# Performance work log

Hardware: AMD Instinct MI355X
Metric: run time of the kernel (lower is better)

The kernel has to match this reference:

```python
import jax, jax.numpy as jnp
import numpy as np
import math

DIM = 96
NUM_HEADS = 8
MLP_RATIO = 4.0

def _coord_encoding(h, w, scale, d_model):
    # matches HierarchicalCoordinateEncoding: per freq i, channels are
    # [sin(cell_y), cos(cell_y), sin(cell_x), cos(cell_x), sin(y), cos(y), sin(x), cos(x)]
    y = jnp.arange(h, dtype=jnp.float32) / (h - 1)
    x = jnp.arange(w, dtype=jnp.float32) / (w - 1)
    yy, xx = jnp.meshgrid(y, x, indexing='ij')
    yf = yy.reshape(-1)
    xf = xx.reshape(-1)
    cs = 2.0 / scale
    coords4 = jnp.stack([yf * cs, xf * cs, yf, xf], axis=-1)  # [N,4]
    nf = d_model // 8
    freqs = (2.0 ** jnp.arange(nf, dtype=jnp.float32)) * math.pi  # [nf]
    phase = coords4[:, None, :] * freqs[None, :, None]  # [N,nf,4]
    enc = jnp.stack([jnp.sin(phase), jnp.cos(phase)], axis=-1)  # [N,nf,4,2]
    return enc.reshape(h * w, nf * 8)  # [N,d_model] (d_model divisible by 8)

def _layernorm(x, g, b, eps=1e-5):
    mu = jnp.mean(x, axis=-1, keepdims=True)
    var = jnp.var(x, axis=-1, keepdims=True)
    return (x - mu) * jax.lax.rsqrt(var + eps) * g + b

def setup_inputs():
    key = jax.random.key(0)
    ks = jax.random.split(key, 8)
    B, C, H, W = 8, DIM, 96, 96
    hid = int(DIM * MLP_RATIO)
    std = 0.02
    return {
        'features': jax.random.normal(ks[0], (B, C, H, W), jnp.float32),
        'scale': 2,
        'mlp1_w1': jax.random.normal(ks[1], (2 * DIM, hid), jnp.float32) * std,
        'mlp1_b1': jnp.zeros((hid,), jnp.float32),
        'mlp1_w2': jax.random.normal(ks[2], (hid, DIM), jnp.float32) * std,
        'mlp1_b2': jnp.zeros((DIM,), jnp.float32),
        'norm1_g': jnp.ones((DIM,), jnp.float32),
        'norm1_b': jnp.zeros((DIM,), jnp.float32),
        'qkv_w': jax.random.normal(ks[3], (DIM, 3 * DIM), jnp.float32) * std,
        'proj_w': jax.random.normal(ks[4], (DIM, DIM), jnp.float32) * std,
        'proj_b': jnp.zeros((DIM,), jnp.float32),
        'norm2_g': jnp.ones((DIM,), jnp.float32),
        'norm2_b': jnp.zeros((DIM,), jnp.float32),
        'mlp2_w1': jax.random.normal(ks[5], (DIM, hid), jnp.float32) * std,
        'mlp2_b1': jnp.zeros((hid,), jnp.float32),
        'mlp2_w2': jax.random.normal(ks[6], (hid, 3), jnp.float32) * std,
        'mlp2_b2': jnp.zeros((3,), jnp.float32),
    }

def reference(features, scale, mlp1_w1, mlp1_b1, mlp1_w2, mlp1_b2, norm1_g, norm1_b, qkv_w, proj_w, proj_b, norm2_g, norm2_b, mlp2_w1, mlp2_b1, mlp2_w2, mlp2_b2):
    B, C, H_lr, W_lr = features.shape
    H, W = int(H_lr * scale), int(W_lr * scale)
    N = H * W
    nh = NUM_HEADS
    hd = C // nh
    ce = _coord_encoding(H, W, float(scale), C)  # [N,C]
    # bilinear upsample, half-pixel centers == torch align_corners=False
    feat_up = jax.image.resize(features, (B, C, H, W), method='linear')
    feat_flat = feat_up.transpose(0, 2, 3, 1).reshape(B, N, C)
    combined = jnp.concatenate([feat_flat, jnp.broadcast_to(ce[None], (B, N, C))], axis=-1)  # [B,N,2C]
    x = jax.nn.gelu(combined @ mlp1_w1 + mlp1_b1, approximate=False) @ mlp1_w2 + mlp1_b2  # [B,N,C]
    x = _layernorm(x, norm1_g, norm1_b)
    # linear attention: softmax over q feature dim and k token dim
    qkv = (x @ qkv_w).reshape(B, N, 3, nh, hd).transpose(2, 0, 3, 1, 4)  # [3,B,nh,N,hd]
    q, k, v = qkv[0], qkv[1], qkv[2]
    q = jax.nn.softmax(q, axis=-1) * (hd ** -0.5)
    k = jax.nn.softmax(k, axis=-2)
    ctx = jnp.einsum('bhnd,bhne->bhde', k, v)  # [B,nh,hd,hd]
    attn = jnp.einsum('bhnd,bhde->bhne', q, ctx)  # [B,nh,N,hd]
    attn = attn.transpose(0, 2, 1, 3).reshape(B, N, C)
    x = x + (attn @ proj_w + proj_b)
    x = _layernorm(x, norm2_g, norm2_b)
    rgb = jax.nn.gelu(x @ mlp2_w1 + mlp2_b1, approximate=False) @ mlp2_w2 + mlp2_b2  # [B,N,3]
    rgb = rgb.reshape(B, H, W, 3).transpose(0, 3, 1, 2)  # [B,3,H,W]
    return jnp.clip(jnp.tanh(rgb) * 0.5 + 0.5, 0.0, 1.0)
```

## Files before the change

kernel.cpp:

```cpp
#include <hip/hip_runtime.h>
#include <math.h>

typedef unsigned short u16;
typedef unsigned int   u32;
typedef unsigned long long u64;
typedef __bf16  bf16x8 __attribute__((ext_vector_type(8)));
typedef short   s16x8  __attribute__((ext_vector_type(8)));
typedef float   f32x4  __attribute__((ext_vector_type(4)));

#define NTOK 36864
#define TTOT (8*NTOK)

__device__ __forceinline__ f32x4 mfma16(s16x8 a, s16x8 b, f32x4 c){
  return __builtin_amdgcn_mfma_f32_16x16x32_bf16(
      __builtin_bit_cast(bf16x8, a), __builtin_bit_cast(bf16x8, b), c, 0, 0, 0);
}
__device__ __forceinline__ int swz(int row, int bc, int stride){
  return row*stride + (bc ^ ((row&7)<<4));
}
__device__ __forceinline__ u16 f2bf(float f){
  u32 u = __float_as_uint(f);
  return (u16)((u + 0x7fffu + ((u>>16)&1u)) >> 16);
}
__device__ __forceinline__ u32 pk2f(float a, float b){
  return (u32)f2bf(a) | ((u32)f2bf(b)<<16);
}
__device__ __forceinline__ u64 pk4f(float a, float b, float c, float d){
  return (u64)pk2f(a,b) | ((u64)pk2f(c,d)<<32);
}
__device__ __forceinline__ float bf2f(u16 h){ return __uint_as_float(((u32)h)<<16); }
__device__ __forceinline__ float rcp_(float x){ return __builtin_amdgcn_rcpf(x); }

__device__ __forceinline__ float gelu_(float x){
  float z = fabsf(x) * 0.70710678118654752f;
  float t = rcp_(1.0f + 0.3275911f*z);
  float poly = t*(0.254829592f + t*(-0.284496736f + t*(1.421413741f + t*(-1.453152027f + t*1.061405429f))));
  float e = __expf(-z*z);
  float erf = 1.0f - poly*e;
  erf = (x < 0.0f) ? -erf : erf;
  return 0.5f*x*(1.0f + erf);
}
__device__ __forceinline__ float tanhf_(float x){
  float e = __expf(2.0f*x);
  return 1.0f - 2.0f*rcp_(e + 1.0f);
}

#define LDSF(arr, row, kc, stride) (*(const s16x8*)((const char*)(arr) + swz((row),(kc)*2,(stride))))

__global__ void prep_w(const float* __restrict__ w1, const float* __restrict__ w2,
                       const float* __restrict__ qkvw, const float* __restrict__ projw,
                       const float* __restrict__ m2w1, const float* __restrict__ m2w2,
                       u16* __restrict__ w1t, u16* __restrict__ w2t,
                       u16* __restrict__ wqt, u16* __restrict__ wkt, u16* __restrict__ wvt,
                       u16* __restrict__ pjt, u16* __restrict__ m2w1t, u16* __restrict__ m2w2t)
{
  int i = blockIdx.x*256 + threadIdx.x;
  if (i < 73728){ int n=i/192, k=i%192; w1t[i] = f2bf(w1[k*384+n]); return; }
  i -= 73728;
  if (i < 36864){ int n=i/384, k=i%384; w2t[i] = f2bf(w2[k*96+n]); return; }
  i -= 36864;
  if (i < 9216){ int n=i/96, k=i%96; wqt[i] = f2bf(qkvw[k*288+n]); return; }
  i -= 9216;
  if (i < 9216){ int n=i/96, k=i%96; wkt[i] = f2bf(qkvw[k*288+96+n]); return; }
  i -= 9216;
  if (i < 9216){ int n=i/96, k=i%96; wvt[i] = f2bf(qkvw[k*288+192+n]); return; }
  i -= 9216;
  if (i < 9216){ int n=i/96, k=i%96; pjt[i] = f2bf(projw[k*96+n]); return; }
  i -= 9216;
  if (i < 36864){ int n=i/96, k=i%96; m2w1t[i] = f2bf(m2w1[k*384+n]); return; }
  i -= 36864;
  if (i < 6144){ int n=i/384, k=i%384; m2w2t[i] = (n<3)? f2bf(m2w2[k*3+n]) : (u16)0; return; }
}

__global__ void prep_feat(const float* __restrict__ feat, u16* __restrict__ featcl){
  __shared__ u16 t[96*100];
  const int tid = threadIdx.x;
  const int b = blockIdx.x/96, y = blockIdx.x%96;
  for (int i=tid; i<9216; i+=256){
    int c = i/96, x = i%96;
    t[c*100+x] = f2bf(feat[((size_t)(b*96+c)*96 + y)*96 + x]);
  }
  __syncthreads();
  for (int i=tid; i<9216; i+=256){
    int x = i/96, c = i%96;
    featcl[(((size_t)b*96 + y)*96 + x)*96 + c] = t[c*100+x];
  }
}

__global__ void prep_ce(u16* __restrict__ ce){
  int gid = blockIdx.x*256 + threadIdx.x;
  if (gid >= 36864*48) return;
  int n = gid/48, c2 = gid%48;
  int row = n/192, col = n%192;
  int fi = c2>>2, cs = c2&3;
  float coord = ((cs&1)==0) ? (float)row*(1.0f/191.0f) : (float)col*(1.0f/191.0f);
  float u = coord * (float)(1<<fi);
  u = u - 2.0f*floorf(u*0.5f);
  float ph = u * 3.14159265358979323846f;
  float s, c;
  __sincosf(ph, &s, &c);
  *(u32*)(ce + (size_t)n*96 + c2*2) = pk2f(s, c);
}

__global__ __launch_bounds__(256,3) void k1(
    const u16* __restrict__ featcl, const u16* __restrict__ ce,
    const u16* __restrict__ w1t, const float* __restrict__ b1,
    const u16* __restrict__ w2t, const float* __restrict__ b2,
    const float* __restrict__ g1, const float* __restrict__ be1,
    const u16* __restrict__ wkt, const u16* __restrict__ wvt,
    u16* __restrict__ x1, float* __restrict__ ctx_un)
{
  __shared__ u16 comb[64*192];
  __shared__ char scratch[26624];
  const int tid = threadIdx.x, w = tid>>6, lane = tid&63, kg = lane>>4, ln = lane&15;
  const int bi = blockIdx.x;
  const int b = bi/576, rem = bi%576, ty = rem/24, tx = rem%24;
  u16* hid  = (u16*)scratch;
  u16* ektp = (u16*)scratch;
  u16* vtp  = (u16*)(scratch + 12288);

  for (int i=tid; i<1024; i+=256){
    int rr = 96 + (i>>6), t = i&63;
    *(u16*)((char*)vtp + swz(rr, t*2, 128)) = (rr==96) ? (u16)0x3f80 : (u16)0;
  }

  {
    const u16* fbase = featcl + (size_t)b*884736;
    const int l = tid>>2, cg = tid&3;
    int row = ty*8 + (l>>3), col = tx*8 + (l&7);
    float fy = row*0.5f - 0.25f;
    int y0 = (int)floorf(fy); float dy = fy - (float)y0;
    int y0c = max(y0,0), y1c = min(y0+1,95);
    float fx = col*0.5f - 0.25f;
    int x0 = (int)floorf(fx); float dx = fx - (float)x0;
    int x0c = max(x0,0), x1c = min(x0+1,95);
    float w00=(1.f-dy)*(1.f-dx), w01=(1.f-dy)*dx, w10=dy*(1.f-dx), w11=dy*dx;
    const u16* p00 = fbase + (size_t)(y0c*96+x0c)*96;
    const u16* p01 = fbase + (size_t)(y0c*96+x1c)*96;
    const u16* p10 = fbase + (size_t)(y1c*96+x0c)*96;
    const u16* p11 = fbase + (size_t)(y1c*96+x1c)*96;
    #pragma unroll
    for (int j=0; j<12; ++j){
      int c2 = cg*12 + j;
      u32 u00 = *(const u32*)(p00 + c2*2), u01 = *(const u32*)(p01 + c2*2);
      u32 u10 = *(const u32*)(p10 + c2*2), u11 = *(const u32*)(p11 + c2*2);
      float a0 = w00*bf2f((u16)u00) + w01*bf2f((u16)u01)
               + w10*bf2f((u16)u10) + w11*bf2f((u16)u11);
      float a1 = w00*bf2f((u16)(u00>>16)) + w01*bf2f((u16)(u01>>16))
               + w10*bf2f((u16)(u10>>16)) + w11*bf2f((u16)(u11>>16));
      *(u32*)((char*)comb + swz(l, c2*4, 384)) = pk2f(a0, a1);
    }
  }
  for (int i=tid; i<64*12; i+=256){
    int l = i/12, sg = i%12;
    int n = (ty*8+(l>>3))*192 + tx*8 + (l&7);
    *(s16x8*)((char*)comb + swz(l, 192 + sg*16, 384)) = *(const s16x8*)(ce + (size_t)n*96 + sg*8);
  }
  __syncthreads();

  f32x4 a2[6] = {};
  for (int h=0; h<2; ++h){
    f32x4 acc[3][4] = {};
    #pragma unroll
    for (int ks=0; ks<6; ++ks){
      s16x8 af[3];
      #pragma unroll
      for (int nf=0; nf<3; ++nf)
        af[nf] = *(const s16x8*)(w1t + (size_t)(192*h+48*w+16*nf+ln)*192 + ks*32+8*kg);
      #pragma unroll
      for (int tf=0; tf<4; ++tf){
        s16x8 bfr = LDSF(comb, 16*tf+ln, ks*32+8*kg, 384);
        #pragma unroll
        for (int nf=0; nf<3; ++nf) acc[nf][tf] = mfma16(af[nf], bfr, acc[nf][tf]);
      }
    }
    #pragma unroll
    for (int nf=0; nf<3; ++nf){
      int lc0 = 48*w + 16*nf + 4*kg;
      float4 bb = *(const float4*)(b1 + 192*h + lc0);
      #pragma unroll
      for (int tf=0; tf<4; ++tf){
        int token = 16*tf + ln;
        u64 v = pk4f(gelu_(acc[nf][tf][0]+bb.x), gelu_(acc[nf][tf][1]+bb.y),
                     gelu_(acc[nf][tf][2]+bb.z), gelu_(acc[nf][tf][3]+bb.w));
        *(u64*)((char*)hid + swz(token, lc0*2, 384)) = v;
      }
    }
    __syncthreads();
    #pragma unroll
    for (int ks=0; ks<6; ++ks){
      s16x8 af = LDSF(hid, 16*w+ln, ks*32+8*kg, 384);
      #pragma unroll
      for (int nf=0; nf<6; ++nf){
        s16x8 bfr = *(const s16x8*)(w2t + (size_t)(16*nf+ln)*384 + 192*h + ks*32+8*kg);
        a2[nf] = mfma16(af, bfr, a2[nf]);
      }
    }
    if (h==0) __syncthreads();
  }

  float gg[6], bbv[6];
  #pragma unroll
  for (int nf=0; nf<6; ++nf){
    int col = 16*nf + ln;
    float bias = b2[col];
    gg[nf] = g1[col]; bbv[nf] = be1[col];
    #pragma unroll
    for (int r=0; r<4; ++r) a2[nf][r] += bias;
  }
  __syncthreads();
  #pragma unroll
  for (int r=0; r<4; ++r){
    float s=0.f, sq=0.f;
    #pragma unroll
    for (int nf=0; nf<6; ++nf){ float v=a2[nf][r]; s+=v; sq+=v*v; }
    #pragma unroll
    for (int m=8; m; m>>=1){ s += __shfl_xor(s,m); sq += __shfl_xor(sq,m); }
    float mean = s*(1.f/96.f);
    float var  = sq*(1.f/96.f) - mean*mean;
    float rstd = rsqrtf(var + 1e-5f);
    int trow = 16*w + 4*kg + r;
    #pragma unroll
    for (int nf=0; nf<6; ++nf){
      float o = (a2[nf][r]-mean)*rstd*gg[nf] + bbv[nf];
      *(u16*)((char*)comb + swz(trow, (16*nf+ln)*2, 256)) = f2bf(o);
    }
  }
  __syncthreads();

  for (int i=tid; i<64*12; i+=256){
    int l = i/12, sg = i%12;
    s16x8 v = *(const s16x8*)((const char*)comb + swz(l, sg*16, 256));
    int n = (ty*8+(l>>3))*192 + tx*8 + (l&7);
    *(s16x8*)(x1 + ((size_t)b*NTOK + n)*96 + sg*8) = v;
  }

  {
    f32x4 ka[6] = {}, va[6] = {};
    #pragma unroll
    for (int ks=0; ks<3; ++ks){
      s16x8 xb = LDSF(comb, 16*w+ln, ks*32+8*kg, 256);
      #pragma unroll
      for (int mf=0; mf<6; ++mf){
        s16x8 ak = *(const s16x8*)(wkt + (size_t)(16*mf+ln)*96 + ks*32+8*kg);
        s16x8 av = *(const s16x8*)(wvt + (size_t)(16*mf+ln)*96 + ks*32+8*kg);
        ka[mf] = mfma16(ak, xb, ka[mf]);
        va[mf] = mfma16(av, xb, va[mf]);
      }
    }
    #pragma unroll
    for (int mf=0; mf<6; ++mf){
      #pragma unroll
      for (int r=0; r<4; ++r){
        int d = 16*mf + 4*kg + r;
        int tok = 16*w + ln;
        *(u16*)((char*)ektp + swz(d, tok*2, 128)) = f2bf(__expf(ka[mf][r]));
        *(u16*)((char*)vtp  + swz(d, tok*2, 128)) = f2bf(va[mf][r]);
      }
    }
  }
  __syncthreads();

  {
    const int tmi[20] = {0,0,1,1,1,2,2,3,3,4,4,4,5,5, 0,1,2,3,4,5};
    const int tni[20] = {0,1,0,1,2,1,2,3,4,3,4,5,4,5, 6,6,6,6,6,6};
    f32x4 c5[5] = {};
    #pragma unroll
    for (int t=0; t<20; ++t){
      if (t/5 == w){
        #pragma unroll
        for (int grp=0; grp<2; ++grp){
          s16x8 ea = LDSF(ektp, 16*tmi[t]+ln, 32*grp+8*kg, 128);
          s16x8 vb = LDSF(vtp,  16*tni[t]+ln, 32*grp+8*kg, 128);
          c5[t%5] = mfma16(ea, vb, c5[t%5]);
        }
      }
    }
    #pragma unroll
    for (int t=0; t<20; ++t){
      if (t/5 == w){
        #pragma unroll
        for (int r=0; r<4; ++r){
          int d = 16*tmi[t] + 4*kg + r;
          if (tni[t]==6){
            if (ln==0) atomicAdd(&ctx_un[(b*96+d)*112 + 96], c5[t%5][r]);
          } else {
            int e = 16*tni[t] + ln;
            if (d/12 == e/12) atomicAdd(&ctx_un[(b*96+d)*112 + e], c5[t%5][r]);
          }
        }
      }
    }
  }
}

__global__ void k2c(const float* __restrict__ ctx_un, float* __restrict__ ctxc){
  int i = blockIdx.x*256 + threadIdx.x;
  if (i < 8*1152){
    int b = i/1152, rr = i%1152, h = rr/144, de = rr%144, d = de/12, e = de%12;
    int dg = h*12+d, eg = h*12+e;
    ctxc[i] = ctx_un[(b*96+dg)*112 + eg] / ctx_un[(b*96+dg)*112 + 96];
  }
}

__global__ __launch_bounds__(256,2) void k3(
    const u16* __restrict__ x1, const u16* __restrict__ wqt, const u16* __restrict__ pjt,
    const float* __restrict__ projb, const float* __restrict__ g2, const float* __restrict__ be2,
    const u16* __restrict__ m2w1t, const float* __restrict__ m2b1,
    const u16* __restrict__ m2w2t, const float* __restrict__ m2b2,
    const float* __restrict__ ctxc, float* __restrict__ out)
{
  __shared__ u16 bufA[128*128];
  __shared__ u16 bufB[128*128];
  __shared__ float ctxsh[8*145];
  __shared__ float rgbsh[3][128];
  const int tid = threadIdx.x, w = tid>>6, lane = tid&63, kg = lane>>4, ln = lane&15;
  const int bi = blockIdx.x, b = bi/288;
  const size_t t0 = (size_t)bi*128;
  const int n0 = (bi%288)*128;

  for (int i=tid; i<1152; i+=256){
    int h = i/144, rem = i%144;
    ctxsh[h*145 + rem] = ctxc[b*1152 + i];
  }

  {
    f32x4 q[6][2] = {};
    #pragma unroll
    for (int ks=0; ks<3; ++ks){
      s16x8 af[6];
      #pragma unroll
      for (int nf=0; nf<6; ++nf)
        af[nf] = *(const s16x8*)(wqt + (size_t)(16*nf+ln)*96 + ks*32+8*kg);
      #pragma unroll
      for (int tf=0; tf<2; ++tf){
        s16x8 bfr = *(const s16x8*)(x1 + (t0 + 32*w + 16*tf + ln)*96 + ks*32+8*kg);
        #pragma unroll
        for (int nf=0; nf<6; ++nf) q[nf][tf] = mfma16(af[nf], bfr, q[nf][tf]);
      }
    }
    #pragma unroll
    for (int nf=0; nf<6; ++nf){
      #pragma unroll
      for (int tf=0; tf<2; ++tf){
        int token = 32*w + 16*tf + ln;
        u64 v = pk4f(q[nf][tf][0], q[nf][tf][1], q[nf][tf][2], q[nf][tf][3]);
        *(u64*)((char*)bufA + swz(token, (16*nf+4*kg)*2, 256)) = v;
      }
    }
  }
  __syncthreads();

  const float scl = 0.28867513459481287f;
  for (int p=tid; p<128*8; p+=256){
    int tok = p>>3, h = p&7;
    const float* cb = &ctxsh[h*145];
    float ex[12], ssum = 0.f;
    #pragma unroll
    for (int d=0; d<12; ++d){
      float qv = bf2f(*(const u16*)((const char*)bufA + swz(tok, (h*12+d)*2, 256)));
      ex[d] = __expf(qv); ssum += ex[d];
    }
    float inv = scl*rcp_(ssum);
    float av[12];
    #pragma unroll
    for (int e=0; e<12; ++e){
      float a = 0.f;
      #pragma unroll
      for (int d=0; d<12; ++d) a += ex[d]*cb[d*12+e];
      av[e] = a*inv;
    }
    #pragma unroll
    for (int e2=0; e2<6; e2+=2){
      u64 v = pk4f(av[2*e2], av[2*e2+1], av[2*e2+2], av[2*e2+3]);
      *(u64*)((char*)bufB + swz(tok, (h*12+2*e2)*2, 256)) = v;
    }
  }
  __syncthreads();

  f32x4 p[2][6] = {};
  #pragma unroll
  for (int ks=0; ks<3; ++ks){
    s16x8 a[2];
    #pragma unroll
    for (int mi=0; mi<2; ++mi) a[mi] = LDSF(bufB, 16*(2*w+mi)+ln, ks*32+8*kg, 256);
    #pragma unroll
    for (int nf=0; nf<6; ++nf){
      s16x8 bfr = *(const s16x8*)(pjt + (size_t)(16*nf+ln)*96 + ks*32+8*kg);
      #pragma unroll
      for (int mi=0; mi<2; ++mi) p[mi][nf] = mfma16(a[mi], bfr, p[mi][nf]);
    }
  }
  {
    float gg[6], bbv[6], pb[6];
    #pragma unroll
    for (int nf=0; nf<6; ++nf){
      int col = 16*nf + ln;
      pb[nf] = projb[col]; gg[nf] = g2[col]; bbv[nf] = be2[col];
    }
    #pragma unroll
    for (int mi=0; mi<2; ++mi){
      #pragma unroll
      for (int r=0; r<4; ++r){
        int trow = 16*(2*w+mi)+4*kg+r;
        float vv[6]; float s=0.f, sq=0.f;
        #pragma unroll
        for (int nf=0; nf<6; ++nf){
          float xv = bf2f(x1[(t0 + trow)*96 + 16*nf+ln]);
          float v = p[mi][nf][r] + pb[nf] + xv;
          vv[nf] = v; s += v; sq += v*v;
        }
        #pragma unroll
        for (int m=8; m; m>>=1){ s += __shfl_xor(s,m); sq += __shfl_xor(sq,m); }
        float mean = s*(1.f/96.f);
        float var  = sq*(1.f/96.f) - mean*mean;
        float rstd = rsqrtf(var + 1e-5f);
        #pragma unroll
        for (int nf=0; nf<6; ++nf){
          float o = (vv[nf]-mean)*rstd*gg[nf] + bbv[nf];
          *(u16*)((char*)bufA + swz(trow, (16*nf+ln)*2, 256)) = f2bf(o);
        }
      }
    }
  }

  f32x4 rgb[2] = {};
  for (int nc=0; nc<4; ++nc){
    f32x4 hh[6][2] = {};
    #pragma unroll
    for (int ks=0; ks<3; ++ks){
      s16x8 af[6];
      #pragma unroll
      for (int nf=0; nf<6; ++nf)
        af[nf] = *(const s16x8*)(m2w1t + (size_t)(nc*96+16*nf+ln)*96 + ks*32+8*kg);
      #pragma unroll
      for (int tf=0; tf<2; ++tf){
        s16x8 bfr = LDSF(bufA, 32*w+16*tf+ln, ks*32+8*kg, 256);
        #pragma unroll
        for (int nf=0; nf<6; ++nf) hh[nf][tf] = mfma16(af[nf], bfr, hh[nf][tf]);
      }
    }
    #pragma unroll
    for (int nf=0; nf<6; ++nf){
      int hc0 = nc*96 + 16*nf + 4*kg;
      float4 bb = *(const float4*)(m2b1 + hc0);
      #pragma unroll
      for (int tf=0; tf<2; ++tf){
        int token = 32*w + 16*tf + ln;
        u64 v = pk4f(gelu_(hh[nf][tf][0]+bb.x), gelu_(hh[nf][tf][1]+bb.y),
                     gelu_(hh[nf][tf][2]+bb.z), gelu_(hh[nf][tf][3]+bb.w));
        *(u64*)((char*)bufB + swz(token, (16*nf+4*kg)*2, 256)) = v;
      }
    }
    #pragma unroll
    for (int ks=0; ks<3; ++ks){
      s16x8 bfr = *(const s16x8*)(m2w2t + (size_t)ln*384 + nc*96 + ks*32 + 8*kg);
      #pragma unroll
      for (int mi=0; mi<2; ++mi){
        s16x8 a = LDSF(bufB, 16*(2*w+mi)+ln, ks*32+8*kg, 256);
        rgb[mi] = mfma16(a, bfr, rgb[mi]);
      }
    }
  }
  if (ln < 3){
    float bias = m2b2[ln];
    #pragma unroll
    for (int mi=0; mi<2; ++mi)
      #pragma unroll
      for (int r=0; r<4; ++r){
        int trow = 16*(2*w+mi)+4*kg+r;
        float v = tanhf_(rgb[mi][r] + bias)*0.5f + 0.5f;
        v = fminf(fmaxf(v, 0.f), 1.f);
        rgbsh[ln][trow] = v;
      }
  }
  __syncthreads();
  for (int i=tid; i<384; i+=256){
    int ch = i>>7, t = i&127;
    out[((size_t)(b*3+ch))*NTOK + n0 + t] = rgbsh[ch][t];
  }
}

extern "C" void kernel_launch(void* const* d_in, const int* in_sizes, int n_in,
                              void* d_out, int out_size, void* d_ws, size_t ws_size,
                              hipStream_t stream)
{
  (void)in_sizes; (void)n_in; (void)out_size; (void)ws_size;
  const float* feat  = (const float*)d_in[0];
  const float* m1w1  = (const float*)d_in[2];
  const float* m1b1  = (const float*)d_in[3];
  const float* m1w2  = (const float*)d_in[4];
  const float* m1b2  = (const float*)d_in[5];
  const float* n1g   = (const float*)d_in[6];
  const float* n1b   = (const float*)d_in[7];
  const float* qkvw  = (const float*)d_in[8];
  const float* projw = (const float*)d_in[9];
  const float* projb = (const float*)d_in[10];
  const float* n2g   = (const float*)d_in[11];
  const float* n2b   = (const float*)d_in[12];
  const float* m2w1  = (const float*)d_in[13];
  const float* m2b1  = (const float*)d_in[14];
  const float* m2w2  = (const float*)d_in[15];
  const float* m2b2  = (const float*)d_in[16];
  float* out = (float*)d_out;

  char* p = (char*)d_ws;
  auto bump = [&](size_t bytes)->char*{
    char* r = p;
    p += (bytes + 255) & ~(size_t)255;
    return r;
  };
  u16*  x1     = (u16*) bump((size_t)TTOT*96*2);
  u16*  featcl = (u16*) bump((size_t)8*96*96*96*2);
  u16*  ce     = (u16*) bump((size_t)NTOK*96*2);
  u16*  w1t    = (u16*) bump(73728*2);
  u16*  w2t    = (u16*) bump(36864*2);
  u16*  wqt    = (u16*) bump(9216*2);
  u16*  wkt    = (u16*) bump(9216*2);
  u16*  wvt    = (u16*) bump(9216*2);
  u16*  pjt    = (u16*) bump(9216*2);
  u16*  m2w1t  = (u16*) bump(36864*2);
  u16*  m2w2t  = (u16*) bump(6144*2);
  float* ctx_un= (float*)bump((size_t)8*96*112*4);
  float* ctxc  = (float*)bump((size_t)8*1152*4);

  hipLaunchKernelGGL(prep_w, dim3(744), dim3(256), 0, stream,
                     m1w1, m1w2, qkvw, projw, m2w1, m2w2,
                     w1t, w2t, wqt, wkt, wvt, pjt, m2w1t, m2w2t);
  hipLaunchKernelGGL(prep_feat, dim3(768), dim3(256), 0, stream, feat, featcl);
  hipLaunchKernelGGL(prep_ce, dim3(6912), dim3(256), 0, stream, ce);
  hipMemsetAsync(ctx_un, 0, (size_t)8*96*112*4, stream);
  hipLaunchKernelGGL(k1, dim3(4608), dim3(256), 0, stream,
                     featcl, ce, w1t, m1b1, w2t, m1b2, n1g, n1b, wkt, wvt, x1, ctx_un);
  hipLaunchKernelGGL(k2c, dim3(36), dim3(256), 0, stream, ctx_un, ctxc);
  hipLaunchKernelGGL(k3, dim3(2304), dim3(256), 0, stream,
                     x1, wqt, pjt, projb, n2g, n2b, m2w1t, m2b1, m2w2t, m2b2, ctxc, out);
}
```

Baseline: 498.6 us.

## Make k1 MLP wave-local over token rows to drop barriers and shrink LDS

The first-MLP stage now gives each wave its own 16-token row block. The hidden dimension is processed in four 96-wide chunks, so the GELU intermediate stays wave-private and needs no block barriers. This removes several __syncthreads and cuts shared memory (the hidden buffer shrinks and the K/V transposes are aliased onto the comb buffer), which allows raising launch bounds to 4 blocks per CU. In exchange, each wave now loads all first-layer weight fragments from global/L2 rather than sharing them across the block's token tiles, which adds weight traffic and register pressure.

```diff
diff --git a/kernel.cpp b/kernel.cpp
--- a/kernel.cpp
+++ b/kernel.cpp
@@ -102,7 +102,7 @@
   *(u32*)(ce + (size_t)n*96 + c2*2) = pk2f(s, c);
 }
 
-__global__ __launch_bounds__(256,3) void k1(
+__global__ __launch_bounds__(256,4) void k1(
     const u16* __restrict__ featcl, const u16* __restrict__ ce,
     const u16* __restrict__ w1t, const float* __restrict__ b1,
     const u16* __restrict__ w2t, const float* __restrict__ b2,
@@ -111,18 +111,13 @@
     u16* __restrict__ x1, float* __restrict__ ctx_un)
 {
   __shared__ u16 comb[64*192];
-  __shared__ char scratch[26624];
+  __shared__ u16 hid[64*128];
   const int tid = threadIdx.x, w = tid>>6, lane = tid&63, kg = lane>>4, ln = lane&15;
   const int bi = blockIdx.x;
   const int b = bi/576, rem = bi%576, ty = rem/24, tx = rem%24;
-  u16* hid  = (u16*)scratch;
-  u16* ektp = (u16*)scratch;
-  u16* vtp  = (u16*)(scratch + 12288);
-
-  for (int i=tid; i<1024; i+=256){
-    int rr = 96 + (i>>6), t = i&63;
-    *(u16*)((char*)vtp + swz(rr, t*2, 128)) = (rr==96) ? (u16)0x3f80 : (u16)0;
-  }
+  char* ektB = (char*)comb;
+  char* vtB  = (char*)comb + 12288;
+  char* vhiB = (char*)hid;
 
   {
     const u16* fbase = featcl + (size_t)b*884736;
@@ -151,112 +146,116 @@
       *(u32*)((char*)comb + swz(l, c2*4, 384)) = pk2f(a0, a1);
     }
   }
-  for (int i=tid; i<64*12; i+=256){
-    int l = i/12, sg = i%12;
-    int n = (ty*8+(l>>3))*192 + tx*8 + (l&7);
-    *(s16x8*)((char*)comb + swz(l, 192 + sg*16, 384)) = *(const s16x8*)(ce + (size_t)n*96 + sg*8);
+  {
+    int row = 16*w + (lane>>2);
+    int n = (ty*8+(row>>3))*192 + tx*8 + (row&7);
+    int sg0 = (lane&3)*3;
+    #pragma unroll
+    for (int j=0; j<3; ++j){
+      int sg = sg0+j;
+      *(s16x8*)((char*)comb + swz(row, 192 + sg*16, 384)) = *(const s16x8*)(ce + (size_t)n*96 + sg*8);
+    }
+  }
+
+  f32x4 a2[6] = {};
+  #pragma unroll
+  for (int q=0; q<4; ++q){
+    f32x4 acc[6] = {};
+    #pragma unroll
+    for (int ks=0; ks<6; ++ks){
+      s16x8 bfr = LDSF(comb, 16*w+ln, ks*32+8*kg, 384);
+      #pragma unroll
+      for (int nf=0; nf<6; ++nf){
+        s16x8 af = *(const s16x8*)(w1t + (size_t)(96*q+16*nf+ln)*192 + ks*32+8*kg);
+        acc[nf] = mfma16(af, bfr, acc[nf]);
+      }
+    }
+    #pragma unroll
+    for (int nf=0; nf<6; ++nf){
+      int lc0 = 16*nf + 4*kg;
+      float4 bb = *(const float4*)(b1 + 96*q + lc0);
+      u64 v = pk4f(gelu_(acc[nf][0]+bb.x), gelu_(acc[nf][1]+bb.y),
+                   gelu_(acc[nf][2]+bb.z), gelu_(acc[nf][3]+bb.w));
+      *(u64*)((char*)hid + swz(16*w+ln, lc0*2, 256)) = v;
+    }
+    #pragma unroll
+    for (int ks=0; ks<3; ++ks){
+      s16x8 af = LDSF(hid, 16*w+ln, ks*32+8*kg, 256);
+      #pragma unroll
+      for (int nf=0; nf<6; ++nf){
+        s16x8 bfr = *(const s16x8*)(w2t + (size_t)(16*nf+ln)*384 + 96*q + ks*32+8*kg);
+        a2[nf] = mfma16(af, bfr, a2[nf]);
+      }
+    }
+  }
+
+  {
+    float gg[6], bbv[6];
+    #pragma unroll
+    for (int nf=0; nf<6; ++nf){
+      int col = 16*nf + ln;
+      float bias = b2[col];
+      gg[nf] = g1[col]; bbv[nf] = be1[col];
+      #pragma unroll
+      for (int r=0; r<4; ++r) a2[nf][r] += bias;
+    }
+    #pragma unroll
+    for (int r=0; r<4; ++r){
+      float s=0.f, sq=0.f;
+      #pragma unroll
+      for (int nf=0; nf<6; ++nf){ float v=a2[nf][r]; s+=v; sq+=v*v; }
+      #pragma unroll
+      for (int m=8; m; m>>=1){ s += __shfl_xor(s,m); sq += __shfl_xor(sq,m); }
+      float mean = s*(1.f/96.f);
+      float var  = sq*(1.f/96.f) - mean*mean;
+      float rstd = rsqrtf(var + 1e-5f);
+      int trow = 16*w + 4*kg + r;
+      #pragma unroll
+      for (int nf=0; nf<6; ++nf){
+        float o = (a2[nf][r]-mean)*rstd*gg[nf] + bbv[nf];
+        *(u16*)((char*)comb + swz(trow, (16*nf+ln)*2, 384)) = f2bf(o);
+      }
+    }
+  }
+
+  {
+    int row = 16*w + (lane>>2);
+    int n = (ty*8+(row>>3))*192 + tx*8 + (row&7);
+    int sg0 = (lane&3)*3;
+    #pragma unroll
+    for (int j=0; j<3; ++j){
+      int sg = sg0+j;
+      s16x8 v = *(const s16x8*)((const char*)comb + swz(row, sg*16, 384));
+      *(s16x8*)(x1 + ((size_t)b*NTOK + n)*96 + sg*8) = v;
+    }
+  }
+
+  f32x4 ka[6] = {}, va[6] = {};
+  #pragma unroll
+  for (int ks=0; ks<3; ++ks){
+    s16x8 xb = LDSF(comb, 16*w+ln, ks*32+8*kg, 384);
+    #pragma unroll
+    for (int mf=0; mf<6; ++mf){
+      s16x8 akf = *(const s16x8*)(wkt + (size_t)(16*mf+ln)*96 + ks*32+8*kg);
+      s16x8 avf = *(const s16x8*)(wvt + (size_t)(16*mf+ln)*96 + ks*32+8*kg);
+      ka[mf] = mfma16(akf, xb, ka[mf]);
+      va[mf] = mfma16(avf, xb, va[mf]);
+    }
   }
   __syncthreads();
 
-  f32x4 a2[6] = {};
-  for (int h=0; h<2; ++h){
-    f32x4 acc[3][4] = {};
-    #pragma unroll
-    for (int ks=0; ks<6; ++ks){
-      s16x8 af[3];
-      #pragma unroll
-      for (int nf=0; nf<3; ++nf)
-        af[nf] = *(const s16x8*)(w1t + (size_t)(192*h+48*w+16*nf+ln)*192 + ks*32+8*kg);
-      #pragma unroll
-      for (int tf=0; tf<4; ++tf){
-        s16x8 bfr = LDSF(comb, 16*tf+ln, ks*32+8*kg, 384);
-        #pragma unroll
-        for (int nf=0; nf<3; ++nf) acc[nf][tf] = mfma16(af[nf], bfr, acc[nf][tf]);
-      }
-    }
-    #pragma unroll
-    for (int nf=0; nf<3; ++nf){
-      int lc0 = 48*w + 16*nf + 4*kg;
-      float4 bb = *(const float4*)(b1 + 192*h + lc0);
-      #pragma unroll
-      for (int tf=0; tf<4; ++tf){
-        int token = 16*tf + ln;
-        u64 v = pk4f(gelu_(acc[nf][tf][0]+bb.x), gelu_(acc[nf][tf][1]+bb.y),
-                     gelu_(acc[nf][tf][2]+bb.z), gelu_(acc[nf][tf][3]+bb.w));
-        *(u64*)((char*)hid + swz(token, lc0*2, 384)) = v;
-      }
-    }
-    __syncthreads();
-    #pragma unroll
-    for (int ks=0; ks<6; ++ks){
-      s16x8 af = LDSF(hid, 16*w+ln, ks*32+8*kg, 384);
-      #pragma unroll
-      for (int nf=0; nf<6; ++nf){
-        s16x8 bfr = *(const s16x8*)(w2t + (size_t)(16*nf+ln)*384 + 192*h + ks*32+8*kg);
-        a2[nf] = mfma16(af, bfr, a2[nf]);
-      }
-    }
-    if (h==0) __syncthreads();
-  }
-
-  float gg[6], bbv[6];
+  for (int i=tid; i<1024; i+=256){
+    int rr = i>>6, t = i&63;
+    *(u16*)(vhiB + swz(rr, t*2, 128)) = (rr==0) ? (u16)0x3f80 : (u16)0;
+  }
   #pragma unroll
-  for (int nf=0; nf<6; ++nf){
-    int col = 16*nf + ln;
-    float bias = b2[col];
-    gg[nf] = g1[col]; bbv[nf] = be1[col];
-    #pragma unroll
-    for (int r=0; r<4; ++r) a2[nf][r] += bias;
-  }
-  __syncthreads();
-  #pragma unroll
-  for (int r=0; r<4; ++r){
-    float s=0.f, sq=0.f;
-    #pragma unroll
-    for (int nf=0; nf<6; ++nf){ float v=a2[nf][r]; s+=v; sq+=v*v; }
-    #pragma unroll
-    for (int m=8; m; m>>=1){ s += __shfl_xor(s,m); sq += __shfl_xor(sq,m); }
-    float mean = s*(1.f/96.f);
-    float var  = sq*(1.f/96.f) - mean*mean;
-    float rstd = rsqrtf(var + 1e-5f);
-    int trow = 16*w + 4*kg + r;
-    #pragma unroll
-    for (int nf=0; nf<6; ++nf){
-      float o = (a2[nf][r]-mean)*rstd*gg[nf] + bbv[nf];
-      *(u16*)((char*)comb + swz(trow, (16*nf+ln)*2, 256)) = f2bf(o);
-    }
-  }
-  __syncthreads();
-
-  for (int i=tid; i<64*12; i+=256){
-    int l = i/12, sg = i%12;
-    s16x8 v = *(const s16x8*)((const char*)comb + swz(l, sg*16, 256));
-    int n = (ty*8+(l>>3))*192 + tx*8 + (l&7);
-    *(s16x8*)(x1 + ((size_t)b*NTOK + n)*96 + sg*8) = v;
-  }
-
-  {
-    f32x4 ka[6] = {}, va[6] = {};
-    #pragma unroll
-    for (int ks=0; ks<3; ++ks){
-      s16x8 xb = LDSF(comb, 16*w+ln, ks*32+8*kg, 256);
-      #pragma unroll
-      for (int mf=0; mf<6; ++mf){
-        s16x8 ak = *(const s16x8*)(wkt + (size_t)(16*mf+ln)*96 + ks*32+8*kg);
-        s16x8 av = *(const s16x8*)(wvt + (size_t)(16*mf+ln)*96 + ks*32+8*kg);
-        ka[mf] = mfma16(ak, xb, ka[mf]);
-        va[mf] = mfma16(av, xb, va[mf]);
-      }
-    }
-    #pragma unroll
-    for (int mf=0; mf<6; ++mf){
-      #pragma unroll
-      for (int r=0; r<4; ++r){
-        int d = 16*mf + 4*kg + r;
-        int tok = 16*w + ln;
-        *(u16*)((char*)ektp + swz(d, tok*2, 128)) = f2bf(__expf(ka[mf][r]));
-        *(u16*)((char*)vtp  + swz(d, tok*2, 128)) = f2bf(va[mf][r]);
-      }
+  for (int mf=0; mf<6; ++mf){
+    #pragma unroll
+    for (int r=0; r<4; ++r){
+      int d = 16*mf + 4*kg + r;
+      int tok = 16*w + ln;
+      *(u16*)(ektB + swz(d, tok*2, 128)) = f2bf(__expf(ka[mf][r]));
+      *(u16*)(vtB  + swz(d, tok*2, 128)) = f2bf(va[mf][r]);
     }
   }
   __syncthreads();
@@ -270,8 +269,10 @@
       if (t/5 == w){
         #pragma unroll
         for (int grp=0; grp<2; ++grp){
-          s16x8 ea = LDSF(ektp, 16*tmi[t]+ln, 32*grp+8*kg, 128);
-          s16x8 vb = LDSF(vtp,  16*tni[t]+ln, 32*grp+8*kg, 128);
+          s16x8 ea = *(const s16x8*)(ektB + swz(16*tmi[t]+ln, (32*grp+8*kg)*2, 128));
+          s16x8 vb = (tni[t]==6)
+            ? *(const s16x8*)(vhiB + swz(ln, (32*grp+8*kg)*2, 128))
+            : *(const s16x8*)(vtB  + swz(16*tni[t]+ln, (32*grp+8*kg)*2, 128));
           c5[t%5] = mfma16(ea, vb, c5[t%5]);
         }
       }
```

Result: slower. 722.4 us (+44.9%).

## Split fused MLP1 kernel into hidden-layer and output kernels via chunked global buffer

Applied to the files above, without the earlier changes.

The fused k1 kernel, which computed the MLP1 hidden layer in LDS and then the second GEMM, LayerNorm and K/V context, is split into two kernels. kB computes the GELU hidden activations for 128-token tiles, each block handling half the hidden width, and writes them to a global bf16 buffer. kC reads them back for the second GEMM, LayerNorm and context accumulation. The work is processed two batches at a time so the intermediate buffer stays small enough to stay L2/MALL-resident. This removes the hidden-half loop, its barriers and the big LDS footprint per block, at the cost of extra global traffic for the 384-wide hidden tensor and more kernel launches.

```diff
diff --git a/kernel.cpp b/kernel.cpp
--- a/kernel.cpp
+++ b/kernel.cpp
@@ -102,32 +102,22 @@
   *(u32*)(ce + (size_t)n*96 + c2*2) = pk2f(s, c);
 }
 
-__global__ __launch_bounds__(256,3) void k1(
+__global__ __launch_bounds__(256,3) void kB(
     const u16* __restrict__ featcl, const u16* __restrict__ ce,
     const u16* __restrict__ w1t, const float* __restrict__ b1,
-    const u16* __restrict__ w2t, const float* __restrict__ b2,
-    const float* __restrict__ g1, const float* __restrict__ be1,
-    const u16* __restrict__ wkt, const u16* __restrict__ wvt,
-    u16* __restrict__ x1, float* __restrict__ ctx_un)
+    u16* __restrict__ hidG, int b0)
 {
-  __shared__ u16 comb[64*192];
-  __shared__ char scratch[26624];
+  __shared__ u16 comb[128*192];
   const int tid = threadIdx.x, w = tid>>6, lane = tid&63, kg = lane>>4, ln = lane&15;
   const int bi = blockIdx.x;
-  const int b = bi/576, rem = bi%576, ty = rem/24, tx = rem%24;
-  u16* hid  = (u16*)scratch;
-  u16* ektp = (u16*)scratch;
-  u16* vtp  = (u16*)(scratch + 12288);
-
-  for (int i=tid; i<1024; i+=256){
-    int rr = 96 + (i>>6), t = i&63;
-    *(u16*)((char*)vtp + swz(rr, t*2, 128)) = (rr==96) ? (u16)0x3f80 : (u16)0;
-  }
+  const int bl = bi/576, r2 = bi%576, tile = r2>>1, half = r2&1;
+  const int b = b0 + bl;
+  const int ty = tile/12, tx = tile%12;
 
   {
     const u16* fbase = featcl + (size_t)b*884736;
-    const int l = tid>>2, cg = tid&3;
-    int row = ty*8 + (l>>3), col = tx*8 + (l&7);
+    const int l = tid>>1, cg = tid&1;
+    int row = ty*8 + (l>>4), col = tx*16 + (l&15);
     float fy = row*0.5f - 0.25f;
     int y0 = (int)floorf(fy); float dy = fy - (float)y0;
     int y0c = max(y0,0), y1c = min(y0+1,95);
@@ -140,8 +130,8 @@
     const u16* p10 = fbase + (size_t)(y1c*96+x0c)*96;
     const u16* p11 = fbase + (size_t)(y1c*96+x1c)*96;
     #pragma unroll
-    for (int j=0; j<12; ++j){
-      int c2 = cg*12 + j;
+    for (int j=0; j<24; ++j){
+      int c2 = cg*24 + j;
       u32 u00 = *(const u32*)(p00 + c2*2), u01 = *(const u32*)(p01 + c2*2);
       u32 u10 = *(const u32*)(p10 + c2*2), u11 = *(const u32*)(p11 + c2*2);
       float a0 = w00*bf2f((u16)u00) + w01*bf2f((u16)u01)
@@ -151,52 +141,76 @@
       *(u32*)((char*)comb + swz(l, c2*4, 384)) = pk2f(a0, a1);
     }
   }
-  for (int i=tid; i<64*12; i+=256){
+  for (int i=tid; i<128*12; i+=256){
     int l = i/12, sg = i%12;
+    int n = (ty*8+(l>>4))*192 + tx*16 + (l&15);
+    *(s16x8*)((char*)comb + swz(l, 192 + sg*16, 384)) = *(const s16x8*)(ce + (size_t)n*96 + sg*8);
+  }
+  __syncthreads();
+
+  f32x4 acc[3][8] = {};
+  #pragma unroll
+  for (int ks=0; ks<6; ++ks){
+    s16x8 af[3];
+    #pragma unroll
+    for (int nf=0; nf<3; ++nf)
+      af[nf] = *(const s16x8*)(w1t + (size_t)(192*half + 48*w + 16*nf + ln)*192 + ks*32+8*kg);
+    #pragma unroll
+    for (int tf=0; tf<8; ++tf){
+      s16x8 bfr = LDSF(comb, 16*tf+ln, ks*32+8*kg, 384);
+      #pragma unroll
+      for (int nf=0; nf<3; ++nf) acc[nf][tf] = mfma16(af[nf], bfr, acc[nf][tf]);
+    }
+  }
+  #pragma unroll
+  for (int nf=0; nf<3; ++nf){
+    int hc0 = 192*half + 48*w + 16*nf + 4*kg;
+    float4 bb = *(const float4*)(b1 + hc0);
+    #pragma unroll
+    for (int tf=0; tf<8; ++tf){
+      int l = 16*tf + ln;
+      int n = (ty*8+(l>>4))*192 + tx*16 + (l&15);
+      u64 v = pk4f(gelu_(acc[nf][tf][0]+bb.x), gelu_(acc[nf][tf][1]+bb.y),
+                   gelu_(acc[nf][tf][2]+bb.z), gelu_(acc[nf][tf][3]+bb.w));
+      *(u64*)(hidG + ((size_t)bl*NTOK + n)*384 + hc0) = v;
+    }
+  }
+}
+
+__global__ __launch_bounds__(256,3) void kC(
+    const u16* __restrict__ hidG, const float* __restrict__ b2,
+    const float* __restrict__ g1, const float* __restrict__ be1,
+    const u16* __restrict__ w2t, const u16* __restrict__ wkt, const u16* __restrict__ wvt,
+    u16* __restrict__ x1, float* __restrict__ ctx_un, int b0)
+{
+  __shared__ u16 x1til[64*128];
+  __shared__ char scratch[26624];
+  const int tid = threadIdx.x, w = tid>>6, lane = tid&63, kg = lane>>4, ln = lane&15;
+  const int bi = blockIdx.x;
+  const int bl = bi/576, rem = bi%576, ty = rem/24, tx = rem%24;
+  const int b = b0 + bl;
+  u16* ektp = (u16*)scratch;
+  u16* vtp  = (u16*)(scratch + 12288);
+
+  for (int i=tid; i<1024; i+=256){
+    int rr = 96 + (i>>6), t = i&63;
+    *(u16*)((char*)vtp + swz(rr, t*2, 128)) = (rr==96) ? (u16)0x3f80 : (u16)0;
+  }
+
+  f32x4 a2[6] = {};
+  {
+    int l = 16*w + ln;
     int n = (ty*8+(l>>3))*192 + tx*8 + (l&7);
-    *(s16x8*)((char*)comb + swz(l, 192 + sg*16, 384)) = *(const s16x8*)(ce + (size_t)n*96 + sg*8);
-  }
-  __syncthreads();
-
-  f32x4 a2[6] = {};
-  for (int h=0; h<2; ++h){
-    f32x4 acc[3][4] = {};
-    #pragma unroll
-    for (int ks=0; ks<6; ++ks){
-      s16x8 af[3];
-      #pragma unroll
-      for (int nf=0; nf<3; ++nf)
-        af[nf] = *(const s16x8*)(w1t + (size_t)(192*h+48*w+16*nf+ln)*192 + ks*32+8*kg);
-      #pragma unroll
-      for (int tf=0; tf<4; ++tf){
-        s16x8 bfr = LDSF(comb, 16*tf+ln, ks*32+8*kg, 384);
-        #pragma unroll
-        for (int nf=0; nf<3; ++nf) acc[nf][tf] = mfma16(af[nf], bfr, acc[nf][tf]);
-      }
-    }
-    #pragma unroll
-    for (int nf=0; nf<3; ++nf){
-      int lc0 = 48*w + 16*nf + 4*kg;
-      float4 bb = *(const float4*)(b1 + 192*h + lc0);
-      #pragma unroll
-      for (int tf=0; tf<4; ++tf){
-        int token = 16*tf + ln;
-        u64 v = pk4f(gelu_(acc[nf][tf][0]+bb.x), gelu_(acc[nf][tf][1]+bb.y),
-                     gelu_(acc[nf][tf][2]+bb.z), gelu_(acc[nf][tf][3]+bb.w));
-        *(u64*)((char*)hid + swz(token, lc0*2, 384)) = v;
-      }
-    }
-    __syncthreads();
-    #pragma unroll
-    for (int ks=0; ks<6; ++ks){
-      s16x8 af = LDSF(hid, 16*w+ln, ks*32+8*kg, 384);
+    const u16* hrow = hidG + ((size_t)bl*NTOK + n)*384;
+    #pragma unroll
+    for (int ks=0; ks<12; ++ks){
+      s16x8 af = *(const s16x8*)(hrow + ks*32 + 8*kg);
       #pragma unroll
       for (int nf=0; nf<6; ++nf){
-        s16x8 bfr = *(const s16x8*)(w2t + (size_t)(16*nf+ln)*384 + 192*h + ks*32+8*kg);
+        s16x8 bfr = *(const s16x8*)(w2t + (size_t)(16*nf+ln)*384 + ks*32+8*kg);
         a2[nf] = mfma16(af, bfr, a2[nf]);
       }
     }
-    if (h==0) __syncthreads();
   }
 
   float gg[6], bbv[6];
@@ -208,7 +222,6 @@
     #pragma unroll
     for (int r=0; r<4; ++r) a2[nf][r] += bias;
   }
-  __syncthreads();
   #pragma unroll
   for (int r=0; r<4; ++r){
     float s=0.f, sq=0.f;
@@ -223,14 +236,14 @@
     #pragma unroll
     for (int nf=0; nf<6; ++nf){
       float o = (a2[nf][r]-mean)*rstd*gg[nf] + bbv[nf];
-      *(u16*)((char*)comb + swz(trow, (16*nf+ln)*2, 256)) = f2bf(o);
+      *(u16*)((char*)x1til + swz(trow, (16*nf+ln)*2, 256)) = f2bf(o);
     }
   }
   __syncthreads();
 
   for (int i=tid; i<64*12; i+=256){
     int l = i/12, sg = i%12;
-    s16x8 v = *(const s16x8*)((const char*)comb + swz(l, sg*16, 256));
+    s16x8 v = *(const s16x8*)((const char*)x1til + swz(l, sg*16, 256));
     int n = (ty*8+(l>>3))*192 + tx*8 + (l&7);
     *(s16x8*)(x1 + ((size_t)b*NTOK + n)*96 + sg*8) = v;
   }
@@ -239,7 +252,7 @@
     f32x4 ka[6] = {}, va[6] = {};
     #pragma unroll
     for (int ks=0; ks<3; ++ks){
-      s16x8 xb = LDSF(comb, 16*w+ln, ks*32+8*kg, 256);
+      s16x8 xb = LDSF(x1til, 16*w+ln, ks*32+8*kg, 256);
       #pragma unroll
       for (int mf=0; mf<6; ++mf){
         s16x8 ak = *(const s16x8*)(wkt + (size_t)(16*mf+ln)*96 + ks*32+8*kg);
@@ -523,6 +536,7 @@
   u16*  m2w2t  = (u16*) bump(6144*2);
   float* ctx_un= (float*)bump((size_t)8*96*112*4);
   float* ctxc  = (float*)bump((size_t)8*1152*4);
+  u16*  hidG   = (u16*) bump((size_t)2*NTOK*384*2);
 
   hipLaunchKernelGGL(prep_w, dim3(744), dim3(256), 0, stream,
                      m1w1, m1w2, qkvw, projw, m2w1, m2w2,
@@ -530,8 +544,12 @@
   hipLaunchKernelGGL(prep_feat, dim3(768), dim3(256), 0, stream, feat, featcl);
   hipLaunchKernelGGL(prep_ce, dim3(6912), dim3(256), 0, stream, ce);
   hipMemsetAsync(ctx_un, 0, (size_t)8*96*112*4, stream);
-  hipLaunchKernelGGL(k1, dim3(4608), dim3(256), 0, stream,
-                     featcl, ce, w1t, m1b1, w2t, m1b2, n1g, n1b, wkt, wvt, x1, ctx_un);
+  for (int c = 0; c < 4; ++c){
+    hipLaunchKernelGGL(kB, dim3(1152), dim3(256), 0, stream,
+                       featcl, ce, w1t, m1b1, hidG, 2*c);
+    hipLaunchKernelGGL(kC, dim3(1152), dim3(256), 0, stream,
+                       hidG, m1b2, n1g, n1b, w2t, wkt, wvt, x1, ctx_un, 2*c);
+  }
   hipLaunchKernelGGL(k2c, dim3(36), dim3(256), 0, stream, ctx_un, ctxc);
   hipLaunchKernelGGL(k3, dim3(2304), dim3(256), 0, stream,
                      x1, wqt, pjt, projb, n2g, n2b, m2w1t, m2b1, m2w2t, m2b2, ctxc, out);
```

Measured after the change: 655.5 us. 31.5% more time.

## Apply linear-attention context via MFMA with block-diagonal bf16 context matrix

Applied to the files above, without the earlier changes.

The per-token scalar loop that applied the q softmax and multiplied by each head's 12x12 context is replaced by one MFMA GEMM. k2c now builds a padded bf16 block-diagonal context matrix per batch, pre-scaled, with extra rows of ones so the same GEMM also produces each head's softmax denominator. The denominator is then broadcast with shuffles and applied before the projection. This removes the LDS context staging, the scalar FMA loop and two barriers, at the cost of some wasted MFMA work on zero blocks and the context being rounded to bf16.

```diff
diff --git a/kernel.cpp b/kernel.cpp
--- a/kernel.cpp
+++ b/kernel.cpp
@@ -294,36 +294,39 @@
   }
 }
 
-__global__ void k2c(const float* __restrict__ ctx_un, float* __restrict__ ctxc){
+__global__ void k2c(const float* __restrict__ ctx_un, u16* __restrict__ ctxBG){
   int i = blockIdx.x*256 + threadIdx.x;
-  if (i < 8*1152){
-    int b = i/1152, rr = i%1152, h = rr/144, de = rr%144, d = de/12, e = de%12;
-    int dg = h*12+d, eg = h*12+e;
-    ctxc[i] = ctx_un[(b*96+dg)*112 + eg] / ctx_un[(b*96+dg)*112 + 96];
-  }
+  if (i >= 8*112*128) return;
+  int b = i/14336, rr = i%14336, row = rr/128, d = rr%128;
+  u16 v = 0;
+  if (row < 96){
+    if (d < 96 && d/12 == row/12){
+      float c = ctx_un[(b*96+d)*112 + row] / ctx_un[(b*96+d)*112 + 96];
+      v = f2bf(c * 0.28867513459481287f);
+    }
+  } else {
+    int h = row - 96;
+    if (d < 96 && d/12 == h) v = (u16)0x3f80;
+  }
+  ctxBG[(size_t)b*14336 + row*128 + d] = v;
 }
 
 __global__ __launch_bounds__(256,2) void k3(
-    const u16* __restrict__ x1, const u16* __restrict__ wqt, const u16* __restrict__ pjt,
+    const u16* __restrict__ x1, const u16* __restrict__ wqt, const u16* __restrict__ ctxBG,
+    const u16* __restrict__ pjt,
     const float* __restrict__ projb, const float* __restrict__ g2, const float* __restrict__ be2,
     const u16* __restrict__ m2w1t, const float* __restrict__ m2b1,
     const u16* __restrict__ m2w2t, const float* __restrict__ m2b2,
-    const float* __restrict__ ctxc, float* __restrict__ out)
+    float* __restrict__ out)
 {
   __shared__ u16 bufA[128*128];
   __shared__ u16 bufB[128*128];
-  __shared__ float ctxsh[8*145];
   __shared__ float rgbsh[3][128];
   const int tid = threadIdx.x, w = tid>>6, lane = tid&63, kg = lane>>4, ln = lane&15;
   const int bi = blockIdx.x, b = bi/288;
   const size_t t0 = (size_t)bi*128;
   const int n0 = (bi%288)*128;
 
-  for (int i=tid; i<1152; i+=256){
-    int h = i/144, rem = i%144;
-    ctxsh[h*145 + rem] = ctxc[b*1152 + i];
-  }
-
   {
     f32x4 q[6][2] = {};
     #pragma unroll
@@ -344,41 +347,48 @@
       #pragma unroll
       for (int tf=0; tf<2; ++tf){
         int token = 32*w + 16*tf + ln;
-        u64 v = pk4f(q[nf][tf][0], q[nf][tf][1], q[nf][tf][2], q[nf][tf][3]);
+        u64 v = pk4f(__expf(q[nf][tf][0]), __expf(q[nf][tf][1]),
+                     __expf(q[nf][tf][2]), __expf(q[nf][tf][3]));
         *(u64*)((char*)bufA + swz(token, (16*nf+4*kg)*2, 256)) = v;
       }
     }
   }
-  __syncthreads();
-
-  const float scl = 0.28867513459481287f;
-  for (int p=tid; p<128*8; p+=256){
-    int tok = p>>3, h = p&7;
-    const float* cb = &ctxsh[h*145];
-    float ex[12], ssum = 0.f;
-    #pragma unroll
-    for (int d=0; d<12; ++d){
-      float qv = bf2f(*(const u16*)((const char*)bufA + swz(tok, (h*12+d)*2, 256)));
-      ex[d] = __expf(qv); ssum += ex[d];
-    }
-    float inv = scl*rcp_(ssum);
-    float av[12];
-    #pragma unroll
-    for (int e=0; e<12; ++e){
-      float a = 0.f;
-      #pragma unroll
-      for (int d=0; d<12; ++d) a += ex[d]*cb[d*12+e];
-      av[e] = a*inv;
-    }
-    #pragma unroll
-    for (int e2=0; e2<6; e2+=2){
-      u64 v = pk4f(av[2*e2], av[2*e2+1], av[2*e2+2], av[2*e2+3]);
-      *(u64*)((char*)bufB + swz(tok, (h*12+2*e2)*2, 256)) = v;
-    }
-  }
-  __syncthreads();
-
-  f32x4 p[2][6] = {};
+
+  f32x4 p[2][7] = {};
+  {
+    const u16* cb = ctxBG + (size_t)b*14336;
+    #pragma unroll
+    for (int ks=0; ks<3; ++ks){
+      s16x8 a[2];
+      #pragma unroll
+      for (int mi=0; mi<2; ++mi) a[mi] = LDSF(bufA, 16*(2*w+mi)+ln, ks*32+8*kg, 256);
+      #pragma unroll
+      for (int nf=0; nf<7; ++nf){
+        s16x8 bfr = *(const s16x8*)(cb + (size_t)(16*nf+ln)*128 + ks*32+8*kg);
+        #pragma unroll
+        for (int mi=0; mi<2; ++mi) p[mi][nf] = mfma16(a[mi], bfr, p[mi][nf]);
+      }
+    }
+  }
+  #pragma unroll
+  for (int mi=0; mi<2; ++mi){
+    f32x4 inv;
+    #pragma unroll
+    for (int r=0; r<4; ++r) inv[r] = rcp_(p[mi][6][r]);
+    #pragma unroll
+    for (int nf=0; nf<6; ++nf){
+      int h = (16*nf + ln) / 12;
+      int src = (lane & 0x30) + h;
+      #pragma unroll
+      for (int r=0; r<4; ++r){
+        float iv = __shfl(inv[r], src, 64);
+        int trow = 16*(2*w+mi) + 4*kg + r;
+        *(u16*)((char*)bufB + swz(trow, (16*nf+ln)*2, 256)) = f2bf(p[mi][nf][r] * iv);
+      }
+    }
+  }
+
+  f32x4 pp[2][6] = {};
   #pragma unroll
   for (int ks=0; ks<3; ++ks){
     s16x8 a[2];
@@ -388,7 +398,7 @@
     for (int nf=0; nf<6; ++nf){
       s16x8 bfr = *(const s16x8*)(pjt + (size_t)(16*nf+ln)*96 + ks*32+8*kg);
       #pragma unroll
-      for (int mi=0; mi<2; ++mi) p[mi][nf] = mfma16(a[mi], bfr, p[mi][nf]);
+      for (int mi=0; mi<2; ++mi) pp[mi][nf] = mfma16(a[mi], bfr, pp[mi][nf]);
     }
   }
   {
@@ -407,7 +417,7 @@
         #pragma unroll
         for (int nf=0; nf<6; ++nf){
           float xv = bf2f(x1[(t0 + trow)*96 + 16*nf+ln]);
-          float v = p[mi][nf][r] + pb[nf] + xv;
+          float v = pp[mi][nf][r] + pb[nf] + xv;
           vv[nf] = v; s += v; sq += v*v;
         }
         #pragma unroll
@@ -522,7 +532,7 @@
   u16*  m2w1t  = (u16*) bump(36864*2);
   u16*  m2w2t  = (u16*) bump(6144*2);
   float* ctx_un= (float*)bump((size_t)8*96*112*4);
-  float* ctxc  = (float*)bump((size_t)8*1152*4);
+  u16*  ctxBG  = (u16*) bump((size_t)8*112*128*2);
 
   hipLaunchKernelGGL(prep_w, dim3(744), dim3(256), 0, stream,
                      m1w1, m1w2, qkvw, projw, m2w1, m2w2,
@@ -532,7 +542,7 @@
   hipMemsetAsync(ctx_un, 0, (size_t)8*96*112*4, stream);
   hipLaunchKernelGGL(k1, dim3(4608), dim3(256), 0, stream,
                      featcl, ce, w1t, m1b1, w2t, m1b2, n1g, n1b, wkt, wvt, x1, ctx_un);
-  hipLaunchKernelGGL(k2c, dim3(36), dim3(256), 0, stream, ctx_un, ctxc);
+  hipLaunchKernelGGL(k2c, dim3(448), dim3(256), 0, stream, ctx_un, ctxBG);
   hipLaunchKernelGGL(k3, dim3(2304), dim3(256), 0, stream,
-                     x1, wqt, pjt, projb, n2g, n2b, m2w1t, m2b1, m2w2t, m2b2, ctxc, out);
-}
+                     x1, wqt, ctxBG, pjt, projb, n2g, n2b, m2w1t, m2b1, m2w2t, m2b2, out);
+}
```

New measurement: 496.2 us. No clear change (-0.5%).
